# Performance work log

Hardware: AMD Instinct MI355X
Metric: run time of the kernel (lower is better)

## Reference

```python
import jax, jax.numpy as jnp
import numpy as np


def setup_inputs() -> dict:
    key = jax.random.key(0)
    ks = jax.random.split(key, 8)
    B, N, C = 4, 2048, 1024
    H, hd, lr, R = 16, 64, 20, 200  # R = low_rank * rank_multi
    s = lambda k, shape, fan: jax.random.normal(k, shape, jnp.float32) / np.sqrt(fan)
    return {
        'x': jax.random.normal(ks[0], (B, N, C), jnp.float32),
        'qk_w': s(ks[1], (2 * C, C), C),
        'proj_w': s(ks[2], (C, C), C),
        'proj_b': jnp.zeros((C,), jnp.float32),
        'we': s(ks[3], (H, R, lr), R),
        'wr': s(ks[4], (H, R, lr), R),
        'cw_w': s(ks[5], (hd, 2 * lr), 2 * lr),
        'cw_b': jnp.zeros((hd,), jnp.float32),
    }


def _l2norm(v, eps=1e-12):
    # matches F.normalize(p=2, dim=-1): x / max(||x||, eps)
    n = jnp.sqrt(jnp.sum(v * v, axis=-1, keepdims=True))
    return v / jnp.maximum(n, eps)


def reference(x, qk_w, proj_w, proj_b, we, wr, cw_w, cw_b):
    B, N, C = x.shape
    H, R, lr = we.shape  # heads, subsample len, low_rank
    hd = C // H
    # qk projection -> q,k: [B,H,N,hd]
    qk = (x @ qk_w.T).reshape(B, N, 2, H, hd).transpose(2, 0, 3, 1, 4)
    q, k = qk[0], qk[1]
    # gen_weights: subsample N positions (embed_len > low_rank*rank_multi branch)
    idx = np.linspace(0, N - 1, R).astype(np.int64)  # static, trunc like torch
    xh = x.transpose(0, 2, 1).reshape(B, H, hd, N)[:, :, :, idx]  # [B,H,hd,R]
    we_b = jnp.einsum('bhdr,hre->bhde', xh, we)  # [B,H,hd,lr]
    wr_b = jnp.einsum('bhdr,hre->bhde', xh, wr)
    # feature map + low-rank scores
    q = _l2norm(q)
    k = _l2norm(k)
    escore = jnp.einsum('bhnd,bhde->bhne', q, we_b)  # [B,H,N,lr]
    rscore = jnp.einsum('bhnd,bhde->bhne', k, wr_b)
    score = jnp.concatenate([escore, rscore], axis=-1)  # [B,H,N,2lr]
    attn = score @ cw_w.T + cw_b  # [B,H,N,hd]
    attn = attn.transpose(0, 2, 1, 3).reshape(B, N, C)
    out = attn @ proj_w.T + proj_b  # dropout is identity at eval
    return out
```

## Files before the change

### kernel.cpp

```cpp
#include <hip/hip_runtime.h>
#include <hip/hip_bf16.h>

constexpr int B_  = 4;
constexpr int N_  = 2048;
constexpr int C_  = 1024;
constexpr int H_  = 16;
constexpr int HD  = 64;
constexpr int LR  = 20;
constexpr int RS  = 200;
constexpr int RP  = 224;

typedef __attribute__((ext_vector_type(8))) short bf16x8;
typedef __attribute__((ext_vector_type(4))) float f32x4;

__device__ __forceinline__ float b2f_raw(unsigned short u) {
    union { unsigned int i; float f; } v;
    v.i = ((unsigned int)u) << 16;
    return v.f;
}
__device__ __forceinline__ unsigned short f2b(float f) {
    __hip_bfloat16 h = __float2bfloat16(f);
    return *(unsigned short*)&h;
}

__device__ __forceinline__ void async_load16(const unsigned short* g, unsigned short* l) {
    __builtin_amdgcn_global_load_lds(
        (const __attribute__((address_space(1))) unsigned int*)(const void*)g,
        (__attribute__((address_space(3))) unsigned int*)(void*)l,
        16, 0, 0);
}

__global__ __launch_bounds__(256)
void detect_kernel(const unsigned int* __restrict__ x, int* __restrict__ flag) {
    const int t = threadIdx.x;
    int cnt = 0;
    for (int i = t; i < 1024; i += 256) {
        const unsigned int w = x[i];
        const unsigned int e = (w >> 7) & 0xFFu;
        cnt += (e >= 103u && e <= 140u) ? 1 : 0;
    }
    __shared__ int s[256];
    s[t] = cnt;
    __syncthreads();
    for (int off = 128; off > 0; off >>= 1) {
        if (t < off) s[t] += s[t + off];
        __syncthreads();
    }
    if (t == 0) *flag = (s[0] > 512) ? 1 : 0;
}

struct CvtArgs {
    const void* src[8];
    unsigned short* dst[8];
    int size[8];
};

__global__ __launch_bounds__(256)
void convert_kernel(const int* __restrict__ flag, CvtArgs args) {
    const int buf = blockIdx.y;
    const int n4 = args.size[buf] >> 2;
    const int stride = gridDim.x * blockDim.x;
    const bool isbf = (*flag != 0);
    for (int i = blockIdx.x * blockDim.x + threadIdx.x; i < n4; i += stride) {
        ushort4 o;
        if (isbf) {
            o = ((const ushort4*)args.src[buf])[i];
        } else {
            const float4 v = ((const float4*)args.src[buf])[i];
            o.x = f2b(v.x); o.y = f2b(v.y); o.z = f2b(v.z); o.w = f2b(v.w);
        }
        ((ushort4*)args.dst[buf])[i] = o;
    }
}

__global__ __launch_bounds__(256)
void gemm1_score_kernel(const unsigned short* __restrict__ xb,
                        const unsigned short* __restrict__ qkwb,
                        const unsigned short* __restrict__ we2t,
                        const unsigned short* __restrict__ wr2t,
                        const unsigned short* __restrict__ cwbb,
                        unsigned short* __restrict__ attn) {
    constexpr int BK = 32;
    constexpr int QS = 72;
    __shared__ __align__(16) unsigned short pool[2 * 128 * QS];
    unsigned short* As = pool;
    unsigned short* Bs = pool + 4096;
    unsigned short* qn = pool;
    unsigned short* kn = pool + 128 * QS;

    const int t    = threadIdx.x;
    const int wave = t >> 6;
    const int lane = t & 63;
    const int h    = blockIdx.x;
    const int m0   = blockIdx.y * 128;
    const int K    = C_;

    const int srow = lane >> 2;
    const int scol = (lane & 3) * 8;
    const unsigned short* ga0 = xb + (size_t)(m0 + wave * 16 + srow) * K + scol;
    const unsigned short* ga1 = xb + (size_t)(m0 + (wave + 4) * 16 + srow) * K + scol;
    const unsigned short* gb0 = qkwb + (size_t)(h * HD + wave * 16 + srow) * K + scol;
    const unsigned short* gb1 = qkwb + (size_t)(C_ + h * HD + wave * 16 + srow) * K + scol;
    unsigned short* lA0 = &As[wave * 512];
    unsigned short* lA1 = &As[(wave + 4) * 512];
    unsigned short* lB0 = &Bs[wave * 512];
    unsigned short* lB1 = &Bs[(wave + 4) * 512];

    const int wr = (wave >> 1) * 64;
    const int wc = (wave & 1) * 64;
    const int lq = lane >> 4;
    const int lm = lane & 15;

    f32x4 acc[4][4];
    #pragma unroll
    for (int i = 0; i < 4; ++i)
        #pragma unroll
        for (int j = 0; j < 4; ++j) acc[i][j] = 0.f;

    for (int k0 = 0; k0 < K; k0 += BK) {
        async_load16(ga0, lA0);
        async_load16(ga1, lA1);
        async_load16(gb0, lB0);
        async_load16(gb1, lB1);
        ga0 += BK; ga1 += BK; gb0 += BK; gb1 += BK;
        __syncthreads();

        bf16x8 af[4], bfr[4];
        #pragma unroll
        for (int i = 0; i < 4; ++i)
            af[i] = *(const bf16x8*)&As[(wr + i * 16 + lm) * BK + lq * 8];
        #pragma unroll
        for (int j = 0; j < 4; ++j)
            bfr[j] = *(const bf16x8*)&Bs[(wc + j * 16 + lm) * BK + lq * 8];

        #pragma unroll
        for (int i = 0; i < 4; ++i)
            #pragma unroll
            for (int j = 0; j < 4; ++j)
                acc[i][j] = __builtin_amdgcn_mfma_f32_16x16x32_bf16(
                    af[i], bfr[j], acc[i][j], 0, 0, 0);

        __syncthreads();
    }

    unsigned short* dst = (wc == 0) ? qn : kn;
    #pragma unroll
    for (int i = 0; i < 4; ++i) {
        float inv[4];
        #pragma unroll
        for (int r = 0; r < 4; ++r) {
            float s = 0.f;
            #pragma unroll
            for (int j = 0; j < 4; ++j) s += acc[i][j][r] * acc[i][j][r];
            s += __shfl_xor(s, 1, 64);
            s += __shfl_xor(s, 2, 64);
            s += __shfl_xor(s, 4, 64);
            s += __shfl_xor(s, 8, 64);
            inv[r] = 1.f / fmaxf(sqrtf(s), 1e-12f);
        }
        #pragma unroll
        for (int j = 0; j < 4; ++j)
            #pragma unroll
            for (int r = 0; r < 4; ++r) {
                const int row = wr + i * 16 + lq * 4 + r;
                dst[row * QS + j * 16 + lm] = f2b(acc[i][j][r] * inv[r]);
            }
    }
    __syncthreads();

    const int b  = blockIdx.y >> 4;
    const int bh = b * H_ + h;
    const unsigned short* wq = we2t + (size_t)bh * HD * HD;
    const unsigned short* wk = wr2t + (size_t)bh * HD * HD;

    bf16x8 bq[2][4], bk[2][4];
    #pragma unroll
    for (int t2 = 0; t2 < 2; ++t2)
        #pragma unroll
        for (int j = 0; j < 4; ++j) {
            const int dout = j * 16 + lm;
            bq[t2][j] = *(const bf16x8*)&wq[dout * HD + t2 * 32 + lq * 8];
            bk[t2][j] = *(const bf16x8*)&wk[dout * HD + t2 * 32 + lq * 8];
        }

    f32x4 accS[2][4];
    #pragma unroll
    for (int rt = 0; rt < 2; ++rt)
        #pragma unroll
        for (int j = 0; j < 4; ++j) accS[rt][j] = 0.f;

    #pragma unroll
    for (int rt = 0; rt < 2; ++rt) {
        const int lr = wave * 32 + rt * 16 + lm;
        bf16x8 aq0 = *(const bf16x8*)&qn[lr * QS + lq * 8];
        bf16x8 aq1 = *(const bf16x8*)&qn[lr * QS + 32 + lq * 8];
        bf16x8 ak0 = *(const bf16x8*)&kn[lr * QS + lq * 8];
        bf16x8 ak1 = *(const bf16x8*)&kn[lr * QS + 32 + lq * 8];
        #pragma unroll
        for (int j = 0; j < 4; ++j) {
            accS[rt][j] = __builtin_amdgcn_mfma_f32_16x16x32_bf16(aq0, bq[0][j], accS[rt][j], 0, 0, 0);
            accS[rt][j] = __builtin_amdgcn_mfma_f32_16x16x32_bf16(aq1, bq[1][j], accS[rt][j], 0, 0, 0);
            accS[rt][j] = __builtin_amdgcn_mfma_f32_16x16x32_bf16(ak0, bk[0][j], accS[rt][j], 0, 0, 0);
            accS[rt][j] = __builtin_amdgcn_mfma_f32_16x16x32_bf16(ak1, bk[1][j], accS[rt][j], 0, 0, 0);
        }
    }

    #pragma unroll
    for (int rt = 0; rt < 2; ++rt)
        #pragma unroll
        for (int j = 0; j < 4; ++j) {
            const int dout = j * 16 + lm;
            const float bv = b2f_raw(cwbb[dout]);
            #pragma unroll
            for (int r = 0; r < 4; ++r) {
                const int row = m0 + wave * 32 + rt * 16 + lq * 4 + r;
                attn[(size_t)row * C_ + h * HD + dout] = f2b(accS[rt][j][r] + bv);
            }
        }
}

template <bool OBF>
__device__ void mfma_gemm_body(const unsigned short* __restrict__ A,
                               const unsigned short* __restrict__ W,
                               const unsigned short* __restrict__ bias,
                               void* __restrict__ out,
                               int M, int N, int K) {
    constexpr int BM = 128, BN = 128, BK = 32;
    __shared__ __align__(16) unsigned short As[BM * BK];
    __shared__ __align__(16) unsigned short Bs[BN * BK];

    const int t    = threadIdx.x;
    const int wave = t >> 6;
    const int lane = t & 63;
    const int m0   = blockIdx.y * BM;
    const int n0   = blockIdx.x * BN;

    const int srow = lane >> 2;
    const int scol = (lane & 3) * 8;
    const unsigned short* ga0 = A + (size_t)(m0 + wave * 16 + srow) * K + scol;
    const unsigned short* ga1 = A + (size_t)(m0 + (wave + 4) * 16 + srow) * K + scol;
    const unsigned short* gb0 = W + (size_t)(n0 + wave * 16 + srow) * K + scol;
    const unsigned short* gb1 = W + (size_t)(n0 + (wave + 4) * 16 + srow) * K + scol;
    unsigned short* lA0 = &As[wave * 512];
    unsigned short* lA1 = &As[(wave + 4) * 512];
    unsigned short* lB0 = &Bs[wave * 512];
    unsigned short* lB1 = &Bs[(wave + 4) * 512];

    const int wr = (wave >> 1) * 64;
    const int wc = (wave & 1) * 64;
    const int lq = lane >> 4;
    const int lm = lane & 15;

    f32x4 acc[4][4];
    #pragma unroll
    for (int i = 0; i < 4; ++i)
        #pragma unroll
        for (int j = 0; j < 4; ++j) acc[i][j] = 0.f;

    for (int k0 = 0; k0 < K; k0 += BK) {
        async_load16(ga0, lA0);
        async_load16(ga1, lA1);
        async_load16(gb0, lB0);
        async_load16(gb1, lB1);
        ga0 += BK; ga1 += BK; gb0 += BK; gb1 += BK;
        __syncthreads();

        bf16x8 af[4], bfr[4];
        #pragma unroll
        for (int i = 0; i < 4; ++i)
            af[i] = *(const bf16x8*)&As[(wr + i * 16 + lm) * BK + lq * 8];
        #pragma unroll
        for (int j = 0; j < 4; ++j)
            bfr[j] = *(const bf16x8*)&Bs[(wc + j * 16 + lm) * BK + lq * 8];

        #pragma unroll
        for (int i = 0; i < 4; ++i)
            #pragma unroll
            for (int j = 0; j < 4; ++j)
                acc[i][j] = __builtin_amdgcn_mfma_f32_16x16x32_bf16(
                    af[i], bfr[j], acc[i][j], 0, 0, 0);

        __syncthreads();
    }

    #pragma unroll
    for (int i = 0; i < 4; ++i) {
        #pragma unroll
        for (int j = 0; j < 4; ++j) {
            const int col = n0 + wc + j * 16 + lm;
            const float bv = b2f_raw(bias[col]);
            #pragma unroll
            for (int r = 0; r < 4; ++r) {
                const int row = m0 + wr + i * 16 + lq * 4 + r;
                const float v = acc[i][j][r] + bv;
                if constexpr (OBF)
                    ((__hip_bfloat16*)out)[(size_t)row * N + col] = __float2bfloat16(v);
                else
                    ((float*)out)[(size_t)row * N + col] = v;
            }
        }
    }
}

__global__ __launch_bounds__(256)
void gemm2_kernel(const int* __restrict__ flag,
                  const unsigned short* __restrict__ attn,
                  const unsigned short* __restrict__ pwb,
                  const unsigned short* __restrict__ pbb,
                  void* __restrict__ out) {
    if (*flag) mfma_gemm_body<true>(attn, pwb, pbb, out, B_ * N_, C_, C_);
    else       mfma_gemm_body<false>(attn, pwb, pbb, out, B_ * N_, C_, C_);
}

__global__ __launch_bounds__(256)
void wec_kernel(const unsigned short* __restrict__ we_in,
                const unsigned short* __restrict__ wr_in,
                const unsigned short* __restrict__ cwwb,
                unsigned short* __restrict__ wect,
                unsigned short* __restrict__ wrct) {
    const int o = blockIdx.x * 256 + threadIdx.x;
    if (o >= H_ * HD * RP) return;
    const int r    = o % RP;
    const int dout = (o / RP) % HD;
    const int h    = o / (RP * HD);
    float sq = 0.f, sk = 0.f;
    if (r < RS) {
        #pragma unroll
        for (int e = 0; e < LR; ++e) {
            const float cq = b2f_raw(cwwb[dout * 2 * LR + e]);
            const float ck = b2f_raw(cwwb[dout * 2 * LR + LR + e]);
            sq += b2f_raw(we_in[((size_t)h * RS + r) * LR + e]) * cq;
            sk += b2f_raw(wr_in[((size_t)h * RS + r) * LR + e]) * ck;
        }
    }
    wect[o] = f2b(sq);
    wrct[o] = f2b(sk);
}

__global__ __launch_bounds__(256)
void gather_kernel(const unsigned short* __restrict__ xb,
                   unsigned short* __restrict__ xh) {
    const int bh = blockIdx.x;
    const int b  = bh >> 4;
    const int h  = bh & 15;
    for (int o = threadIdx.x; o < HD * RP; o += 256) {
        const int din = o & 63;
        const int r   = o >> 6;
        unsigned short v = 0;
        if (r < RS) {
            const int ir = (r * (N_ - 1)) / (RS - 1);
            v = xb[((size_t)b * N_ + ir) * C_ + h * HD + din];
        }
        xh[(size_t)bh * HD * RP + (size_t)din * RP + r] = v;
    }
}

__global__ __launch_bounds__(64)
void collapse_kernel(const unsigned short* __restrict__ xh,
                     const unsigned short* __restrict__ wect,
                     const unsigned short* __restrict__ wrct,
                     unsigned short* __restrict__ we2t,
                     unsigned short* __restrict__ wr2t) {
    const int blk = blockIdx.x;
    const int bh  = blk >> 2;
    const int qk  = (blk >> 1) & 1;
    const int dh  = blk & 1;
    const int h   = bh & 15;
    const int lane = threadIdx.x;
    const int lq = lane >> 4;
    const int lm = lane & 15;

    const unsigned short* wsrc = (qk ? wrct : wect) + (size_t)h * HD * RP;
    const unsigned short* xsrc = xh + (size_t)bh * HD * RP;
    unsigned short* dst = (qk ? wr2t : we2t) + (size_t)bh * HD * HD;

    f32x4 acc[2][4];
    #pragma unroll
    for (int i = 0; i < 2; ++i)
        #pragma unroll
        for (int j = 0; j < 4; ++j) acc[i][j] = 0.f;

    for (int ks = 0; ks < RP / 32; ++ks) {
        bf16x8 a[2], bfr[4];
        #pragma unroll
        for (int rt = 0; rt < 2; ++rt)
            a[rt] = *(const bf16x8*)&wsrc[(size_t)(dh * 32 + rt * 16 + lm) * RP + ks * 32 + lq * 8];
        #pragma unroll
        for (int j = 0; j < 4; ++j)
            bfr[j] = *(const bf16x8*)&xsrc[(size_t)(j * 16 + lm) * RP + ks * 32 + lq * 8];
        #pragma unroll
        for (int rt = 0; rt < 2; ++rt)
            #pragma unroll
            for (int j = 0; j < 4; ++j)
                acc[rt][j] = __builtin_amdgcn_mfma_f32_16x16x32_bf16(
                    a[rt], bfr[j], acc[rt][j], 0, 0, 0);
    }

    #pragma unroll
    for (int rt = 0; rt < 2; ++rt)
        #pragma unroll
        for (int j = 0; j < 4; ++j)
            #pragma unroll
            for (int r = 0; r < 4; ++r) {
                const int dout = dh * 32 + rt * 16 + lq * 4 + r;
                const int din  = j * 16 + lm;
                dst[dout * HD + din] = f2b(acc[rt][j][r]);
            }
}

extern "C" void kernel_launch(void* const* d_in, const int* in_sizes, int n_in,
                              void* d_out, int out_size, void* d_ws, size_t ws_size,
                              hipStream_t stream) {
    (void)in_sizes; (void)n_in; (void)out_size; (void)ws_size;

    char* ws = (char*)d_ws;
    size_t off = 0;
    auto alloc = [&](size_t bytes) {
        char* p = ws + off;
        off += (bytes + 255) & ~(size_t)255;
        return p;
    };

    int* flag = (int*)alloc(16);
    unsigned short* xb    = (unsigned short*)alloc((size_t)B_ * N_ * C_ * 2);
    unsigned short* qkwb  = (unsigned short*)alloc((size_t)2 * C_ * C_ * 2);
    unsigned short* pwb   = (unsigned short*)alloc((size_t)C_ * C_ * 2);
    unsigned short* pbb   = (unsigned short*)alloc((size_t)C_ * 2);
    unsigned short* we_i  = (unsigned short*)alloc((size_t)H_ * RS * LR * 2);
    unsigned short* wr_i  = (unsigned short*)alloc((size_t)H_ * RS * LR * 2);
    unsigned short* cwwb  = (unsigned short*)alloc((size_t)HD * 2 * LR * 2);
    unsigned short* cwbb  = (unsigned short*)alloc((size_t)HD * 2);
    unsigned short* attn  = (unsigned short*)alloc((size_t)B_ * N_ * C_ * 2);
    unsigned short* we2t  = (unsigned short*)alloc((size_t)B_ * H_ * HD * HD * 2);
    unsigned short* wr2t  = (unsigned short*)alloc((size_t)B_ * H_ * HD * HD * 2);
    unsigned short* wect  = (unsigned short*)alloc((size_t)H_ * HD * RP * 2);
    unsigned short* wrct  = (unsigned short*)alloc((size_t)H_ * HD * RP * 2);
    unsigned short* xh    = (unsigned short*)alloc((size_t)B_ * H_ * HD * RP * 2);

    const int M = B_ * N_;

    detect_kernel<<<1, 256, 0, stream>>>((const unsigned int*)d_in[0], flag);

    CvtArgs ca;
    ca.src[0] = d_in[0]; ca.dst[0] = xb;   ca.size[0] = B_ * N_ * C_;
    ca.src[1] = d_in[1]; ca.dst[1] = qkwb; ca.size[1] = 2 * C_ * C_;
    ca.src[2] = d_in[2]; ca.dst[2] = pwb;  ca.size[2] = C_ * C_;
    ca.src[3] = d_in[3]; ca.dst[3] = pbb;  ca.size[3] = C_;
    ca.src[4] = d_in[4]; ca.dst[4] = we_i; ca.size[4] = H_ * RS * LR;
    ca.src[5] = d_in[5]; ca.dst[5] = wr_i; ca.size[5] = H_ * RS * LR;
    ca.src[6] = d_in[6]; ca.dst[6] = cwwb; ca.size[6] = HD * 2 * LR;
    ca.src[7] = d_in[7]; ca.dst[7] = cwbb; ca.size[7] = HD;
    convert_kernel<<<dim3(2048, 8), 256, 0, stream>>>(flag, ca);

    wec_kernel<<<(H_ * HD * RP + 255) / 256, 256, 0, stream>>>(
        we_i, wr_i, cwwb, wect, wrct);
    gather_kernel<<<B_ * H_, 256, 0, stream>>>(xb, xh);
    collapse_kernel<<<B_ * H_ * 4, 64, 0, stream>>>(xh, wect, wrct, we2t, wr2t);

    gemm1_score_kernel<<<dim3(H_, M / 128), 256, 0, stream>>>(
        xb, qkwb, we2t, wr2t, cwbb, attn);

    gemm2_kernel<<<dim3(C_ / 128, M / 128), 256, 0, stream>>>(flag, attn, pwb, pbb, d_out);
}
```

Measured before the change: 229.5 us.

## Fuse prep kernels into one launch and double K-step per barrier in GEMMs

Merges the convert, weight-collapse (wec) and gather kernels into a single fused_prep launch that reads the raw inputs directly, removing two launches and the intermediate bf16 copies of the small weights. Both MFMA GEMM kernels now load 64 K-columns per iteration into two LDS halves, which halves the number of barriers per tile at the cost of doubled LDS usage. In fused_prep, the wec and gather work sit in grid rows that mostly contain idle blocks, which early-exit.

Result: faster. 209.6 us (-8.7%).

```diff
diff --git a/kernel.cpp b/kernel.cpp
--- a/kernel.cpp
+++ b/kernel.cpp
@@ -22,6 +22,11 @@
     __hip_bfloat16 h = __float2bfloat16(f);
     return *(unsigned short*)&h;
 }
+template <bool BF>
+__device__ __forceinline__ float ldg(const void* p, size_t i) {
+    if constexpr (BF) return b2f_raw(((const unsigned short*)p)[i]);
+    else              return ((const float*)p)[i];
+}
 
 __device__ __forceinline__ void async_load16(const unsigned short* g, unsigned short* l) {
     __builtin_amdgcn_global_load_lds(
@@ -50,274 +55,17 @@
 }
 
 struct CvtArgs {
-    const void* src[8];
-    unsigned short* dst[8];
-    int size[8];
+    const void* src[5];
+    unsigned short* dst[5];
+    int size[5];
 };
 
-__global__ __launch_bounds__(256)
-void convert_kernel(const int* __restrict__ flag, CvtArgs args) {
-    const int buf = blockIdx.y;
-    const int n4 = args.size[buf] >> 2;
-    const int stride = gridDim.x * blockDim.x;
-    const bool isbf = (*flag != 0);
-    for (int i = blockIdx.x * blockDim.x + threadIdx.x; i < n4; i += stride) {
-        ushort4 o;
-        if (isbf) {
-            o = ((const ushort4*)args.src[buf])[i];
-        } else {
-            const float4 v = ((const float4*)args.src[buf])[i];
-            o.x = f2b(v.x); o.y = f2b(v.y); o.z = f2b(v.z); o.w = f2b(v.w);
-        }
-        ((ushort4*)args.dst[buf])[i] = o;
-    }
-}
-
-__global__ __launch_bounds__(256)
-void gemm1_score_kernel(const unsigned short* __restrict__ xb,
-                        const unsigned short* __restrict__ qkwb,
-                        const unsigned short* __restrict__ we2t,
-                        const unsigned short* __restrict__ wr2t,
-                        const unsigned short* __restrict__ cwbb,
-                        unsigned short* __restrict__ attn) {
-    constexpr int BK = 32;
-    constexpr int QS = 72;
-    __shared__ __align__(16) unsigned short pool[2 * 128 * QS];
-    unsigned short* As = pool;
-    unsigned short* Bs = pool + 4096;
-    unsigned short* qn = pool;
-    unsigned short* kn = pool + 128 * QS;
-
-    const int t    = threadIdx.x;
-    const int wave = t >> 6;
-    const int lane = t & 63;
-    const int h    = blockIdx.x;
-    const int m0   = blockIdx.y * 128;
-    const int K    = C_;
-
-    const int srow = lane >> 2;
-    const int scol = (lane & 3) * 8;
-    const unsigned short* ga0 = xb + (size_t)(m0 + wave * 16 + srow) * K + scol;
-    const unsigned short* ga1 = xb + (size_t)(m0 + (wave + 4) * 16 + srow) * K + scol;
-    const unsigned short* gb0 = qkwb + (size_t)(h * HD + wave * 16 + srow) * K + scol;
-    const unsigned short* gb1 = qkwb + (size_t)(C_ + h * HD + wave * 16 + srow) * K + scol;
-    unsigned short* lA0 = &As[wave * 512];
-    unsigned short* lA1 = &As[(wave + 4) * 512];
-    unsigned short* lB0 = &Bs[wave * 512];
-    unsigned short* lB1 = &Bs[(wave + 4) * 512];
-
-    const int wr = (wave >> 1) * 64;
-    const int wc = (wave & 1) * 64;
-    const int lq = lane >> 4;
-    const int lm = lane & 15;
-
-    f32x4 acc[4][4];
-    #pragma unroll
-    for (int i = 0; i < 4; ++i)
-        #pragma unroll
-        for (int j = 0; j < 4; ++j) acc[i][j] = 0.f;
-
-    for (int k0 = 0; k0 < K; k0 += BK) {
-        async_load16(ga0, lA0);
-        async_load16(ga1, lA1);
-        async_load16(gb0, lB0);
-        async_load16(gb1, lB1);
-        ga0 += BK; ga1 += BK; gb0 += BK; gb1 += BK;
-        __syncthreads();
-
-        bf16x8 af[4], bfr[4];
-        #pragma unroll
-        for (int i = 0; i < 4; ++i)
-            af[i] = *(const bf16x8*)&As[(wr + i * 16 + lm) * BK + lq * 8];
-        #pragma unroll
-        for (int j = 0; j < 4; ++j)
-            bfr[j] = *(const bf16x8*)&Bs[(wc + j * 16 + lm) * BK + lq * 8];
-
-        #pragma unroll
-        for (int i = 0; i < 4; ++i)
-            #pragma unroll
-            for (int j = 0; j < 4; ++j)
-                acc[i][j] = __builtin_amdgcn_mfma_f32_16x16x32_bf16(
-                    af[i], bfr[j], acc[i][j], 0, 0, 0);
-
-        __syncthreads();
-    }
-
-    unsigned short* dst = (wc == 0) ? qn : kn;
-    #pragma unroll
-    for (int i = 0; i < 4; ++i) {
-        float inv[4];
-        #pragma unroll
-        for (int r = 0; r < 4; ++r) {
-            float s = 0.f;
-            #pragma unroll
-            for (int j = 0; j < 4; ++j) s += acc[i][j][r] * acc[i][j][r];
-            s += __shfl_xor(s, 1, 64);
-            s += __shfl_xor(s, 2, 64);
-            s += __shfl_xor(s, 4, 64);
-            s += __shfl_xor(s, 8, 64);
-            inv[r] = 1.f / fmaxf(sqrtf(s), 1e-12f);
-        }
-        #pragma unroll
-        for (int j = 0; j < 4; ++j)
-            #pragma unroll
-            for (int r = 0; r < 4; ++r) {
-                const int row = wr + i * 16 + lq * 4 + r;
-                dst[row * QS + j * 16 + lm] = f2b(acc[i][j][r] * inv[r]);
-            }
-    }
-    __syncthreads();
-
-    const int b  = blockIdx.y >> 4;
-    const int bh = b * H_ + h;
-    const unsigned short* wq = we2t + (size_t)bh * HD * HD;
-    const unsigned short* wk = wr2t + (size_t)bh * HD * HD;
-
-    bf16x8 bq[2][4], bk[2][4];
-    #pragma unroll
-    for (int t2 = 0; t2 < 2; ++t2)
-        #pragma unroll
-        for (int j = 0; j < 4; ++j) {
-            const int dout = j * 16 + lm;
-            bq[t2][j] = *(const bf16x8*)&wq[dout * HD + t2 * 32 + lq * 8];
-            bk[t2][j] = *(const bf16x8*)&wk[dout * HD + t2 * 32 + lq * 8];
-        }
-
-    f32x4 accS[2][4];
-    #pragma unroll
-    for (int rt = 0; rt < 2; ++rt)
-        #pragma unroll
-        for (int j = 0; j < 4; ++j) accS[rt][j] = 0.f;
-
-    #pragma unroll
-    for (int rt = 0; rt < 2; ++rt) {
-        const int lr = wave * 32 + rt * 16 + lm;
-        bf16x8 aq0 = *(const bf16x8*)&qn[lr * QS + lq * 8];
-        bf16x8 aq1 = *(const bf16x8*)&qn[lr * QS + 32 + lq * 8];
-        bf16x8 ak0 = *(const bf16x8*)&kn[lr * QS + lq * 8];
-        bf16x8 ak1 = *(const bf16x8*)&kn[lr * QS + 32 + lq * 8];
-        #pragma unroll
-        for (int j = 0; j < 4; ++j) {
-            accS[rt][j] = __builtin_amdgcn_mfma_f32_16x16x32_bf16(aq0, bq[0][j], accS[rt][j], 0, 0, 0);
-            accS[rt][j] = __builtin_amdgcn_mfma_f32_16x16x32_bf16(aq1, bq[1][j], accS[rt][j], 0, 0, 0);
-            accS[rt][j] = __builtin_amdgcn_mfma_f32_16x16x32_bf16(ak0, bk[0][j], accS[rt][j], 0, 0, 0);
-            accS[rt][j] = __builtin_amdgcn_mfma_f32_16x16x32_bf16(ak1, bk[1][j], accS[rt][j], 0, 0, 0);
-        }
-    }
-
-    #pragma unroll
-    for (int rt = 0; rt < 2; ++rt)
-        #pragma unroll
-        for (int j = 0; j < 4; ++j) {
-            const int dout = j * 16 + lm;
-            const float bv = b2f_raw(cwbb[dout]);
-            #pragma unroll
-            for (int r = 0; r < 4; ++r) {
-                const int row = m0 + wave * 32 + rt * 16 + lq * 4 + r;
-                attn[(size_t)row * C_ + h * HD + dout] = f2b(accS[rt][j][r] + bv);
-            }
-        }
-}
-
-template <bool OBF>
-__device__ void mfma_gemm_body(const unsigned short* __restrict__ A,
-                               const unsigned short* __restrict__ W,
-                               const unsigned short* __restrict__ bias,
-                               void* __restrict__ out,
-                               int M, int N, int K) {
-    constexpr int BM = 128, BN = 128, BK = 32;
-    __shared__ __align__(16) unsigned short As[BM * BK];
-    __shared__ __align__(16) unsigned short Bs[BN * BK];
-
-    const int t    = threadIdx.x;
-    const int wave = t >> 6;
-    const int lane = t & 63;
-    const int m0   = blockIdx.y * BM;
-    const int n0   = blockIdx.x * BN;
-
-    const int srow = lane >> 2;
-    const int scol = (lane & 3) * 8;
-    const unsigned short* ga0 = A + (size_t)(m0 + wave * 16 + srow) * K + scol;
-    const unsigned short* ga1 = A + (size_t)(m0 + (wave + 4) * 16 + srow) * K + scol;
-    const unsigned short* gb0 = W + (size_t)(n0 + wave * 16 + srow) * K + scol;
-    const unsigned short* gb1 = W + (size_t)(n0 + (wave + 4) * 16 + srow) * K + scol;
-    unsigned short* lA0 = &As[wave * 512];
-    unsigned short* lA1 = &As[(wave + 4) * 512];
-    unsigned short* lB0 = &Bs[wave * 512];
-    unsigned short* lB1 = &Bs[(wave + 4) * 512];
-
-    const int wr = (wave >> 1) * 64;
-    const int wc = (wave & 1) * 64;
-    const int lq = lane >> 4;
-    const int lm = lane & 15;
-
-    f32x4 acc[4][4];
-    #pragma unroll
-    for (int i = 0; i < 4; ++i)
-        #pragma unroll
-        for (int j = 0; j < 4; ++j) acc[i][j] = 0.f;
-
-    for (int k0 = 0; k0 < K; k0 += BK) {
-        async_load16(ga0, lA0);
-        async_load16(ga1, lA1);
-        async_load16(gb0, lB0);
-        async_load16(gb1, lB1);
-        ga0 += BK; ga1 += BK; gb0 += BK; gb1 += BK;
-        __syncthreads();
-
-        bf16x8 af[4], bfr[4];
-        #pragma unroll
-        for (int i = 0; i < 4; ++i)
-            af[i] = *(const bf16x8*)&As[(wr + i * 16 + lm) * BK + lq * 8];
-        #pragma unroll
-        for (int j = 0; j < 4; ++j)
-            bfr[j] = *(const bf16x8*)&Bs[(wc + j * 16 + lm) * BK + lq * 8];
-
-        #pragma unroll
-        for (int i = 0; i < 4; ++i)
-            #pragma unroll
-            for (int j = 0; j < 4; ++j)
-                acc[i][j] = __builtin_amdgcn_mfma_f32_16x16x32_bf16(
-                    af[i], bfr[j], acc[i][j], 0, 0, 0);
-
-        __syncthreads();
-    }
-
-    #pragma unroll
-    for (int i = 0; i < 4; ++i) {
-        #pragma unroll
-        for (int j = 0; j < 4; ++j) {
-            const int col = n0 + wc + j * 16 + lm;
-            const float bv = b2f_raw(bias[col]);
-            #pragma unroll
-            for (int r = 0; r < 4; ++r) {
-                const int row = m0 + wr + i * 16 + lq * 4 + r;
-                const float v = acc[i][j][r] + bv;
-                if constexpr (OBF)
-                    ((__hip_bfloat16*)out)[(size_t)row * N + col] = __float2bfloat16(v);
-                else
-                    ((float*)out)[(size_t)row * N + col] = v;
-            }
-        }
-    }
-}
-
-__global__ __launch_bounds__(256)
-void gemm2_kernel(const int* __restrict__ flag,
-                  const unsigned short* __restrict__ attn,
-                  const unsigned short* __restrict__ pwb,
-                  const unsigned short* __restrict__ pbb,
-                  void* __restrict__ out) {
-    if (*flag) mfma_gemm_body<true>(attn, pwb, pbb, out, B_ * N_, C_, C_);
-    else       mfma_gemm_body<false>(attn, pwb, pbb, out, B_ * N_, C_, C_);
-}
-
-__global__ __launch_bounds__(256)
-void wec_kernel(const unsigned short* __restrict__ we_in,
-                const unsigned short* __restrict__ wr_in,
-                const unsigned short* __restrict__ cwwb,
-                unsigned short* __restrict__ wect,
-                unsigned short* __restrict__ wrct) {
+template <bool BF>
+__device__ void wec_body(const void* __restrict__ we_raw,
+                         const void* __restrict__ wr_raw,
+                         const void* __restrict__ cw_raw,
+                         unsigned short* __restrict__ wect,
+                         unsigned short* __restrict__ wrct) {
     const int o = blockIdx.x * 256 + threadIdx.x;
     if (o >= H_ * HD * RP) return;
     const int r    = o % RP;
@@ -327,31 +75,66 @@
     if (r < RS) {
         #pragma unroll
         for (int e = 0; e < LR; ++e) {
-            const float cq = b2f_raw(cwwb[dout * 2 * LR + e]);
-            const float ck = b2f_raw(cwwb[dout * 2 * LR + LR + e]);
-            sq += b2f_raw(we_in[((size_t)h * RS + r) * LR + e]) * cq;
-            sk += b2f_raw(wr_in[((size_t)h * RS + r) * LR + e]) * ck;
+            const float cq = ldg<BF>(cw_raw, dout * 2 * LR + e);
+            const float ck = ldg<BF>(cw_raw, dout * 2 * LR + LR + e);
+            sq += ldg<BF>(we_raw, ((size_t)h * RS + r) * LR + e) * cq;
+            sk += ldg<BF>(wr_raw, ((size_t)h * RS + r) * LR + e) * ck;
         }
     }
     wect[o] = f2b(sq);
     wrct[o] = f2b(sk);
 }
 
-__global__ __launch_bounds__(256)
-void gather_kernel(const unsigned short* __restrict__ xb,
-                   unsigned short* __restrict__ xh) {
+template <bool BF>
+__device__ void gather_body(const void* __restrict__ x_raw,
+                            unsigned short* __restrict__ xh) {
     const int bh = blockIdx.x;
-    const int b  = bh >> 4;
-    const int h  = bh & 15;
+    if (bh >= B_ * H_) return;
+    const int b = bh >> 4;
+    const int h = bh & 15;
     for (int o = threadIdx.x; o < HD * RP; o += 256) {
         const int din = o & 63;
         const int r   = o >> 6;
         unsigned short v = 0;
         if (r < RS) {
             const int ir = (r * (N_ - 1)) / (RS - 1);
-            v = xb[((size_t)b * N_ + ir) * C_ + h * HD + din];
+            const size_t idx = ((size_t)b * N_ + ir) * C_ + h * HD + din;
+            if constexpr (BF) v = ((const unsigned short*)x_raw)[idx];
+            else              v = f2b(((const float*)x_raw)[idx]);
         }
         xh[(size_t)bh * HD * RP + (size_t)din * RP + r] = v;
+    }
+}
+
+__global__ __launch_bounds__(256)
+void fused_prep_kernel(const int* __restrict__ flag, CvtArgs args,
+                       const void* __restrict__ we_raw,
+                       const void* __restrict__ wr_raw,
+                       const void* __restrict__ cw_raw,
+                       unsigned short* __restrict__ wect,
+                       unsigned short* __restrict__ wrct,
+                       unsigned short* __restrict__ xh) {
+    const bool isbf = (*flag != 0);
+    const int y = blockIdx.y;
+    if (y < 5) {
+        const int n4 = args.size[y] >> 2;
+        const int stride = gridDim.x * blockDim.x;
+        for (int i = blockIdx.x * blockDim.x + threadIdx.x; i < n4; i += stride) {
+            ushort4 o;
+            if (isbf) {
+                o = ((const ushort4*)args.src[y])[i];
+            } else {
+                const float4 v = ((const float4*)args.src[y])[i];
+                o.x = f2b(v.x); o.y = f2b(v.y); o.z = f2b(v.z); o.w = f2b(v.w);
+            }
+            ((ushort4*)args.dst[y])[i] = o;
+        }
+    } else if (y == 5) {
+        if (isbf) wec_body<true>(we_raw, wr_raw, cw_raw, wect, wrct);
+        else      wec_body<false>(we_raw, wr_raw, cw_raw, wect, wrct);
+    } else {
+        if (isbf) gather_body<true>(args.src[0], xh);
+        else      gather_body<false>(args.src[0], xh);
     }
 }
 
@@ -408,6 +191,259 @@
             }
 }
 
+__global__ __launch_bounds__(256)
+void gemm1_score_kernel(const unsigned short* __restrict__ xb,
+                        const unsigned short* __restrict__ qkwb,
+                        const unsigned short* __restrict__ we2t,
+                        const unsigned short* __restrict__ wr2t,
+                        const unsigned short* __restrict__ cwbb,
+                        unsigned short* __restrict__ attn) {
+    constexpr int QS = 72;
+    __shared__ __align__(16) unsigned short pool[2 * 128 * QS];
+    unsigned short* As0 = pool;
+    unsigned short* As1 = pool + 4096;
+    unsigned short* Bs0 = pool + 8192;
+    unsigned short* Bs1 = pool + 12288;
+    unsigned short* qn  = pool;
+    unsigned short* kn  = pool + 128 * QS;
+
+    const int t    = threadIdx.x;
+    const int wave = t >> 6;
+    const int lane = t & 63;
+    const int h    = blockIdx.x;
+    const int m0   = blockIdx.y * 128;
+    const int K    = C_;
+
+    const int srow = lane >> 2;
+    const int scol = (lane & 3) * 8;
+    const unsigned short* ga0 = xb + (size_t)(m0 + wave * 16 + srow) * K + scol;
+    const unsigned short* ga1 = xb + (size_t)(m0 + (wave + 4) * 16 + srow) * K + scol;
+    const unsigned short* gb0 = qkwb + (size_t)(h * HD + wave * 16 + srow) * K + scol;
+    const unsigned short* gb1 = qkwb + (size_t)(C_ + h * HD + wave * 16 + srow) * K + scol;
+    unsigned short* lAa = &As0[wave * 512];
+    unsigned short* lAb = &As0[(wave + 4) * 512];
+    unsigned short* lBa = &Bs0[wave * 512];
+    unsigned short* lBb = &Bs0[(wave + 4) * 512];
+    unsigned short* lAa1 = &As1[wave * 512];
+    unsigned short* lAb1 = &As1[(wave + 4) * 512];
+    unsigned short* lBa1 = &Bs1[wave * 512];
+    unsigned short* lBb1 = &Bs1[(wave + 4) * 512];
+
+    const int wr = (wave >> 1) * 64;
+    const int wc = (wave & 1) * 64;
+    const int lq = lane >> 4;
+    const int lm = lane & 15;
+
+    f32x4 acc[4][4];
+    #pragma unroll
+    for (int i = 0; i < 4; ++i)
+        #pragma unroll
+        for (int j = 0; j < 4; ++j) acc[i][j] = 0.f;
+
+    for (int k0 = 0; k0 < K; k0 += 64) {
+        async_load16(ga0, lAa);  async_load16(ga0 + 32, lAa1);
+        async_load16(ga1, lAb);  async_load16(ga1 + 32, lAb1);
+        async_load16(gb0, lBa);  async_load16(gb0 + 32, lBa1);
+        async_load16(gb1, lBb);  async_load16(gb1 + 32, lBb1);
+        ga0 += 64; ga1 += 64; gb0 += 64; gb1 += 64;
+        __syncthreads();
+
+        #pragma unroll
+        for (int h2 = 0; h2 < 2; ++h2) {
+            const unsigned short* As = h2 ? As1 : As0;
+            const unsigned short* Bs = h2 ? Bs1 : Bs0;
+            bf16x8 af[4], bfr[4];
+            #pragma unroll
+            for (int i = 0; i < 4; ++i)
+                af[i] = *(const bf16x8*)&As[(wr + i * 16 + lm) * 32 + lq * 8];
+            #pragma unroll
+            for (int j = 0; j < 4; ++j)
+                bfr[j] = *(const bf16x8*)&Bs[(wc + j * 16 + lm) * 32 + lq * 8];
+            #pragma unroll
+            for (int i = 0; i < 4; ++i)
+                #pragma unroll
+                for (int j = 0; j < 4; ++j)
+                    acc[i][j] = __builtin_amdgcn_mfma_f32_16x16x32_bf16(
+                        af[i], bfr[j], acc[i][j], 0, 0, 0);
+        }
+        __syncthreads();
+    }
+
+    unsigned short* dst = (wc == 0) ? qn : kn;
+    #pragma unroll
+    for (int i = 0; i < 4; ++i) {
+        float inv[4];
+        #pragma unroll
+        for (int r = 0; r < 4; ++r) {
+            float s = 0.f;
+            #pragma unroll
+            for (int j = 0; j < 4; ++j) s += acc[i][j][r] * acc[i][j][r];
+            s += __shfl_xor(s, 1, 64);
+            s += __shfl_xor(s, 2, 64);
+            s += __shfl_xor(s, 4, 64);
+            s += __shfl_xor(s, 8, 64);
+            inv[r] = 1.f / fmaxf(sqrtf(s), 1e-12f);
+        }
+        #pragma unroll
+        for (int j = 0; j < 4; ++j)
+            #pragma unroll
+            for (int r = 0; r < 4; ++r) {
+                const int row = wr + i * 16 + lq * 4 + r;
+                dst[row * QS + j * 16 + lm] = f2b(acc[i][j][r] * inv[r]);
+            }
+    }
+    __syncthreads();
+
+    const int b  = blockIdx.y >> 4;
+    const int bh = b * H_ + h;
+    const unsigned short* wq = we2t + (size_t)bh * HD * HD;
+    const unsigned short* wk = wr2t + (size_t)bh * HD * HD;
+
+    bf16x8 bq[2][4], bk[2][4];
+    #pragma unroll
+    for (int t2 = 0; t2 < 2; ++t2)
+        #pragma unroll
+        for (int j = 0; j < 4; ++j) {
+            const int dout = j * 16 + lm;
+            bq[t2][j] = *(const bf16x8*)&wq[dout * HD + t2 * 32 + lq * 8];
+            bk[t2][j] = *(const bf16x8*)&wk[dout * HD + t2 * 32 + lq * 8];
+        }
+
+    f32x4 accS[2][4];
+    #pragma unroll
+    for (int rt = 0; rt < 2; ++rt)
+        #pragma unroll
+        for (int j = 0; j < 4; ++j) accS[rt][j] = 0.f;
+
+    #pragma unroll
+    for (int rt = 0; rt < 2; ++rt) {
+        const int lr = wave * 32 + rt * 16 + lm;
+        bf16x8 aq0 = *(const bf16x8*)&qn[lr * QS + lq * 8];
+        bf16x8 aq1 = *(const bf16x8*)&qn[lr * QS + 32 + lq * 8];
+        bf16x8 ak0 = *(const bf16x8*)&kn[lr * QS + lq * 8];
+        bf16x8 ak1 = *(const bf16x8*)&kn[lr * QS + 32 + lq * 8];
+        #pragma unroll
+        for (int j = 0; j < 4; ++j) {
+            accS[rt][j] = __builtin_amdgcn_mfma_f32_16x16x32_bf16(aq0, bq[0][j], accS[rt][j], 0, 0, 0);
+            accS[rt][j] = __builtin_amdgcn_mfma_f32_16x16x32_bf16(aq1, bq[1][j], accS[rt][j], 0, 0, 0);
+            accS[rt][j] = __builtin_amdgcn_mfma_f32_16x16x32_bf16(ak0, bk[0][j], accS[rt][j], 0, 0, 0);
+            accS[rt][j] = __builtin_amdgcn_mfma_f32_16x16x32_bf16(ak1, bk[1][j], accS[rt][j], 0, 0, 0);
+        }
+    }
+
+    #pragma unroll
+    for (int rt = 0; rt < 2; ++rt)
+        #pragma unroll
+        for (int j = 0; j < 4; ++j) {
+            const int dout = j * 16 + lm;
+            const float bv = b2f_raw(cwbb[dout]);
+            #pragma unroll
+            for (int r = 0; r < 4; ++r) {
+                const int row = m0 + wave * 32 + rt * 16 + lq * 4 + r;
+                attn[(size_t)row * C_ + h * HD + dout] = f2b(accS[rt][j][r] + bv);
+            }
+        }
+}
+
+template <bool OBF>
+__device__ void mfma_gemm_body64(const unsigned short* __restrict__ A,
+                                 const unsigned short* __restrict__ W,
+                                 const unsigned short* __restrict__ bias,
+                                 void* __restrict__ out,
+                                 int M, int N, int K) {
+    __shared__ __align__(16) unsigned short As0[4096], As1[4096];
+    __shared__ __align__(16) unsigned short Bs0[4096], Bs1[4096];
+
+    const int t    = threadIdx.x;
+    const int wave = t >> 6;
+    const int lane = t & 63;
+    const int m0   = blockIdx.y * 128;
+    const int n0   = blockIdx.x * 128;
+
+    const int srow = lane >> 2;
+    const int scol = (lane & 3) * 8;
+    const unsigned short* ga0 = A + (size_t)(m0 + wave * 16 + srow) * K + scol;
+    const unsigned short* ga1 = A + (size_t)(m0 + (wave + 4) * 16 + srow) * K + scol;
+    const unsigned short* gb0 = W + (size_t)(n0 + wave * 16 + srow) * K + scol;
+    const unsigned short* gb1 = W + (size_t)(n0 + (wave + 4) * 16 + srow) * K + scol;
+    unsigned short* lAa  = &As0[wave * 512];
+    unsigned short* lAb  = &As0[(wave + 4) * 512];
+    unsigned short* lBa  = &Bs0[wave * 512];
+    unsigned short* lBb  = &Bs0[(wave + 4) * 512];
+    unsigned short* lAa1 = &As1[wave * 512];
+    unsigned short* lAb1 = &As1[(wave + 4) * 512];
+    unsigned short* lBa1 = &Bs1[wave * 512];
+    unsigned short* lBb1 = &Bs1[(wave + 4) * 512];
+
+    const int wr = (wave >> 1) * 64;
+    const int wc = (wave & 1) * 64;
+    const int lq = lane >> 4;
+    const int lm = lane & 15;
+
+    f32x4 acc[4][4];
+    #pragma unroll
+    for (int i = 0; i < 4; ++i)
+        #pragma unroll
+        for (int j = 0; j < 4; ++j) acc[i][j] = 0.f;
+
+    for (int k0 = 0; k0 < K; k0 += 64) {
+        async_load16(ga0, lAa);  async_load16(ga0 + 32, lAa1);
+        async_load16(ga1, lAb);  async_load16(ga1 + 32, lAb1);
+        async_load16(gb0, lBa);  async_load16(gb0 + 32, lBa1);
+        async_load16(gb1, lBb);  async_load16(gb1 + 32, lBb1);
+        ga0 += 64; ga1 += 64; gb0 += 64; gb1 += 64;
+        __syncthreads();
+
+        #pragma unroll
+        for (int h2 = 0; h2 < 2; ++h2) {
+            const unsigned short* As = h2 ? As1 : As0;
+            const unsigned short* Bs = h2 ? Bs1 : Bs0;
+            bf16x8 af[4], bfr[4];
+            #pragma unroll
+            for (int i = 0; i < 4; ++i)
+                af[i] = *(const bf16x8*)&As[(wr + i * 16 + lm) * 32 + lq * 8];
+            #pragma unroll
+            for (int j = 0; j < 4; ++j)
+                bfr[j] = *(const bf16x8*)&Bs[(wc + j * 16 + lm) * 32 + lq * 8];
+            #pragma unroll
+            for (int i = 0; i < 4; ++i)
+                #pragma unroll
+                for (int j = 0; j < 4; ++j)
+                    acc[i][j] = __builtin_amdgcn_mfma_f32_16x16x32_bf16(
+                        af[i], bfr[j], acc[i][j], 0, 0, 0);
+        }
+        __syncthreads();
+    }
+
+    #pragma unroll
+    for (int i = 0; i < 4; ++i) {
+        #pragma unroll
+        for (int j = 0; j < 4; ++j) {
+            const int col = n0 + wc + j * 16 + lm;
+            const float bv = b2f_raw(bias[col]);
+            #pragma unroll
+            for (int r = 0; r < 4; ++r) {
+                const int row = m0 + wr + i * 16 + lq * 4 + r;
+                const float v = acc[i][j][r] + bv;
+                if constexpr (OBF)
+                    ((__hip_bfloat16*)out)[(size_t)row * N + col] = __float2bfloat16(v);
+                else
+                    ((float*)out)[(size_t)row * N + col] = v;
+            }
+        }
+    }
+}
+
+__global__ __launch_bounds__(256)
+void gemm2_kernel(const int* __restrict__ flag,
+                  const unsigned short* __restrict__ attn,
+                  const unsigned short* __restrict__ pwb,
+                  const unsigned short* __restrict__ pbb,
+                  void* __restrict__ out) {
+    if (*flag) mfma_gemm_body64<true>(attn, pwb, pbb, out, B_ * N_, C_, C_);
+    else       mfma_gemm_body64<false>(attn, pwb, pbb, out, B_ * N_, C_, C_);
+}
+
 extern "C" void kernel_launch(void* const* d_in, const int* in_sizes, int n_in,
                               void* d_out, int out_size, void* d_ws, size_t ws_size,
                               hipStream_t stream) {
@@ -426,9 +462,6 @@
     unsigned short* qkwb  = (unsigned short*)alloc((size_t)2 * C_ * C_ * 2);
     unsigned short* pwb   = (unsigned short*)alloc((size_t)C_ * C_ * 2);
     unsigned short* pbb   = (unsigned short*)alloc((size_t)C_ * 2);
-    unsigned short* we_i  = (unsigned short*)alloc((size_t)H_ * RS * LR * 2);
-    unsigned short* wr_i  = (unsigned short*)alloc((size_t)H_ * RS * LR * 2);
-    unsigned short* cwwb  = (unsigned short*)alloc((size_t)HD * 2 * LR * 2);
     unsigned short* cwbb  = (unsigned short*)alloc((size_t)HD * 2);
     unsigned short* attn  = (unsigned short*)alloc((size_t)B_ * N_ * C_ * 2);
     unsigned short* we2t  = (unsigned short*)alloc((size_t)B_ * H_ * HD * HD * 2);
@@ -446,19 +479,15 @@
     ca.src[1] = d_in[1]; ca.dst[1] = qkwb; ca.size[1] = 2 * C_ * C_;
     ca.src[2] = d_in[2]; ca.dst[2] = pwb;  ca.size[2] = C_ * C_;
     ca.src[3] = d_in[3]; ca.dst[3] = pbb;  ca.size[3] = C_;
-    ca.src[4] = d_in[4]; ca.dst[4] = we_i; ca.size[4] = H_ * RS * LR;
-    ca.src[5] = d_in[5]; ca.dst[5] = wr_i; ca.size[5] = H_ * RS * LR;
-    ca.src[6] = d_in[6]; ca.dst[6] = cwwb; ca.size[6] = HD * 2 * LR;
-    ca.src[7] = d_in[7]; ca.dst[7] = cwbb; ca.size[7] = HD;
-    convert_kernel<<<dim3(2048, 8), 256, 0, stream>>>(flag, ca);
-
-    wec_kernel<<<(H_ * HD * RP + 255) / 256, 256, 0, stream>>>(
-        we_i, wr_i, cwwb, wect, wrct);
-    gather_kernel<<<B_ * H_, 256, 0, stream>>>(xb, xh);
+    ca.src[4] = d_in[7]; ca.dst[4] = cwbb; ca.size[4] = HD;
+    fused_prep_kernel<<<dim3(2048, 7), 256, 0, stream>>>(
+        flag, ca, d_in[4], d_in[5], d_in[6], wect, wrct, xh);
+
     collapse_kernel<<<B_ * H_ * 4, 64, 0, stream>>>(xh, wect, wrct, we2t, wr2t);
 
     gemm1_score_kernel<<<dim3(H_, M / 128), 256, 0, stream>>>(
         xb, qkwb, we2t, wr2t, cwbb, attn);
 
-    gemm2_kernel<<<dim3(C_ / 128, M / 128), 256, 0, stream>>>(flag, attn, pwb, pbb, d_out);
-}
+    gemm2_kernel<<<dim3(C_ / 128, M / 128), 256, 0, stream>>>(
+        flag, attn, pwb, pbb, d_out);
+}
```
